# Kernel optimization log

Measured on AMD Instinct MI355X. Metric: run time of the kernel, lower is better.

Reference implementation:

```python
import jax, jax.numpy as jnp
import numpy as np
import math

N_HEADS = 16
DIM_MODEL = 1024
DIM_KQ = 64
DIM_V = 64
B, T = 2, 2048


def setup_inputs() -> dict:
    key = jax.random.key(0)
    ks = jax.random.split(key, 9)
    s = 1.0 / math.sqrt(DIM_MODEL)
    return {
        "x": jax.random.normal(ks[0], (B, T, DIM_MODEL), dtype=jnp.float32),
        "Wq": jax.random.normal(ks[1], (DIM_MODEL, N_HEADS * DIM_KQ), dtype=jnp.float32) * s,
        "bq": jnp.zeros((N_HEADS * DIM_KQ,), dtype=jnp.float32),
        "Wk": jax.random.normal(ks[2], (DIM_MODEL, N_HEADS * DIM_KQ), dtype=jnp.float32) * s,
        "bk": jnp.zeros((N_HEADS * DIM_KQ,), dtype=jnp.float32),
        "Wv": jax.random.normal(ks[3], (DIM_MODEL, N_HEADS * DIM_V), dtype=jnp.float32) * s,
        "bv": jnp.zeros((N_HEADS * DIM_V,), dtype=jnp.float32),
        "Wo": jax.random.normal(ks[4], (N_HEADS * DIM_V, DIM_MODEL), dtype=jnp.float32) * s,
        "bo": jnp.zeros((DIM_MODEL,), dtype=jnp.float32),
    }


def reference(x, Wq, bq, Wk, bk, Wv, bv, Wo, bo):
    b, t, _ = x.shape
    # projections, split into heads: [B, T, h, d]
    q = (x @ Wq + bq).reshape(b, t, N_HEADS, DIM_KQ)
    k = (x @ Wk + bk).reshape(b, t, N_HEADS, DIM_KQ)
    v = (x @ Wv + bv).reshape(b, t, N_HEADS, DIM_V)
    # NOTE: faithful to source einsum 'B Tq h d, B Tk h d -> B h Tk Tq'
    # scores[b, h, tk, tq] = q[b, tq] . k[b, tk]
    scores = jnp.einsum('bqhd,bkhd->bhkq', q, k)
    # softmax over the LAST axis (= query axis tq), as in the source
    attn = jax.nn.softmax(scores / math.sqrt(DIM_KQ), axis=-1)
    # source einsum 'B h Tk Tq, B Tq h dv -> B Tq h dv':
    # sums over Tk only -> out[b, tq, h, dv] = v[b, tq, h, dv] * sum_tk attn[b, h, tk, tq]
    colsum = attn.sum(axis=2)                      # [B, h, Tq]
    mixed = v * colsum.transpose(0, 2, 1)[..., None]  # [B, Tq, h, dv]
    out = mixed.reshape(b, t, N_HEADS * DIM_V) @ Wo + bo
    return out
```

## Files before the change

kernel.cpp:

```cpp
#include <hip/hip_runtime.h>
#include <hip/hip_bf16.h>
#include <stdint.h>

typedef __attribute__((ext_vector_type(4))) float f32x4;
typedef __attribute__((ext_vector_type(8))) __bf16 bf16x8;

#define AS1 __attribute__((address_space(1)))
#define AS3 __attribute__((address_space(3)))

#if __has_builtin(__builtin_amdgcn_exp2f)
#define EXP2(x) __builtin_amdgcn_exp2f(x)
#else
#define EXP2(x) exp2f(x)
#endif

__device__ __forceinline__ ushort f2bf(float f) {
  uint32_t u = __builtin_bit_cast(uint32_t, f);
  u += 0x7fffu + ((u >> 16) & 1u);
  return (ushort)(u >> 16);
}
__device__ __forceinline__ float bf2f(ushort h) {
  uint32_t u = ((uint32_t)h) << 16;
  return __builtin_bit_cast(float, u);
}

#define SCK 0.18033688011112042f

#define GLD(src, dst) \
  __builtin_amdgcn_global_load_lds((const AS1 uint32_t*)(src), (AS3 uint32_t*)(dst), 16, 0, 0)

#define BARRIER()                          \
  do {                                     \
    __builtin_amdgcn_sched_barrier(0);     \
    __builtin_amdgcn_s_barrier();          \
    __builtin_amdgcn_sched_barrier(0);     \
  } while (0)


__global__ void k_cvt_x(const float* __restrict__ x, ushort* __restrict__ xb, int n4) {
  int i = blockIdx.x * blockDim.x + threadIdx.x;
  if (i >= n4) return;
  float4 v = ((const float4*)x)[i];
  ushort4 o;
  o.x = f2bf(v.x); o.y = f2bf(v.y); o.z = f2bf(v.z); o.w = f2bf(v.w);
  ((ushort4*)xb)[i] = o;
}

__global__ void k_prep_w(const float* __restrict__ Wq, const float* __restrict__ Wk,
                         const float* __restrict__ Wv, const float* __restrict__ Wo,
                         ushort* __restrict__ Wt, ushort* __restrict__ Wot) {
  __shared__ float tile[32][33];
  int z = blockIdx.z;
  const float* src = (z == 0) ? Wq : (z == 1) ? Wk : (z == 2) ? Wv : Wo;
  ushort* dst = (z < 3) ? (Wt + (size_t)z * 1048576) : Wot;
  float scale = (z == 1) ? SCK : 1.0f;
  int k0 = blockIdx.y * 32, n0 = blockIdx.x * 32;
  int tx = threadIdx.x, ty = threadIdx.y;
#pragma unroll
  for (int i = 0; i < 4; i++)
    tile[ty + i * 8][tx] = src[(size_t)(k0 + ty + i * 8) * 1024 + n0 + tx];
  __syncthreads();
#pragma unroll
  for (int i = 0; i < 4; i++)
    dst[(size_t)(n0 + ty + i * 8) * 1024 + k0 + tx] = f2bf(tile[tx][ty + i * 8] * scale);
}

template <int MODE>
__global__ __launch_bounds__(512, 2) void k_gemm8(const ushort* __restrict__ A,
                                                  const ushort* __restrict__ Bt,
                                                  void* __restrict__ Cv,
                                                  const float* __restrict__ b0,
                                                  const float* __restrict__ b1,
                                                  const float* __restrict__ b2,
                                                  int K, int ldc) {
  __shared__ char ldsb[131072];
  const int tid = threadIdx.x;
  const int lane = tid & 63;
  const int wid = tid >> 6;
  const int wr = wid >> 2, wc = wid & 3;
  const int l15 = lane & 15, l4 = lane >> 4;
  const int row0 = blockIdx.y * 256;
  const int col0 = blockIdx.x * 256;
  const int T = K >> 5;

  const int swz = ((tid & 3) ^ ((tid >> 3) & 3)) << 3;
  const ushort* Ap = A + (size_t)(row0 + (tid >> 2)) * K + swz;
  const ushort* Bp = Bt + (size_t)(col0 + (tid >> 2)) * K + swz;

#define STAGE_H1(t)                              \
  do {                                           \
    char* bufs = ldsb + (((t) & 3) << 15);       \
    const ushort* pa = Ap + (size_t)(t) * 32;    \
    GLD(pa, bufs + tid * 16);                    \
    GLD(pa + 128 * K, bufs + 8192 + tid * 16);   \
  } while (0)
#define STAGE_H2(t)                              \
  do {                                           \
    char* bufs = ldsb + (((t) & 3) << 15);       \
    const ushort* pb = Bp + (size_t)(t) * 32;    \
    GLD(pb, bufs + 16384 + tid * 16);            \
    GLD(pb + 128 * K, bufs + 24576 + tid * 16);  \
  } while (0)

  int aoffL[8], boffL[4];
#pragma unroll
  for (int m = 0; m < 8; m++) {
    int r = wr * 128 + m * 16 + l15;
    aoffL[m] = r * 64 + ((l4 ^ ((r >> 1) & 3)) << 4);
  }
#pragma unroll
  for (int n = 0; n < 4; n++) {
    int r = wc * 64 + n * 16 + l15;
    boffL[n] = 16384 + r * 64 + ((l4 ^ ((r >> 1) & 3)) << 4);
  }

  f32x4 acc[8][4] = {};

  STAGE_H1(0); STAGE_H2(0);
  STAGE_H1(1); STAGE_H2(1);
  STAGE_H1(2); STAGE_H2(2);
  asm volatile("s_waitcnt vmcnt(8)" ::: "memory");
  BARRIER();

#define PHASE(t, DO_STAGE, VMSTR)                                                     \
  do {                                                                                \
    char* buf = ldsb + (((t) & 3) << 15);                                             \
    {                                                                                 \
      bf16x8 af[4], bfr[4];                                                           \
      _Pragma("unroll") for (int m = 0; m < 4; m++)                                   \
          af[m] = *(const bf16x8*)(buf + aoffL[m]);                                   \
      _Pragma("unroll") for (int n = 0; n < 4; n++)                                   \
          bfr[n] = *(const bf16x8*)(buf + boffL[n]);                                  \
      if (DO_STAGE) STAGE_H1((t) + 3);                                                \
      BARRIER();                                                                      \
      __builtin_amdgcn_s_setprio(1);                                                  \
      _Pragma("unroll") for (int m = 0; m < 4; m++)                                   \
          _Pragma("unroll") for (int n = 0; n < 4; n++)                               \
              acc[m][n] = __builtin_amdgcn_mfma_f32_16x16x32_bf16(af[m], bfr[n],      \
                                                                  acc[m][n], 0, 0, 0);\
      __builtin_amdgcn_s_setprio(0);                                                  \
      BARRIER();                                                                      \
      bf16x8 af2[4];                                                                  \
      _Pragma("unroll") for (int m = 0; m < 4; m++)                                   \
          af2[m] = *(const bf16x8*)(buf + aoffL[m + 4]);                              \
      if (DO_STAGE) STAGE_H2((t) + 3);                                                \
      BARRIER();                                                                      \
      __builtin_amdgcn_s_setprio(1);                                                  \
      _Pragma("unroll") for (int m = 0; m < 4; m++)                                   \
          _Pragma("unroll") for (int n = 0; n < 4; n++)                               \
              acc[m + 4][n] = __builtin_amdgcn_mfma_f32_16x16x32_bf16(                \
                  af2[m], bfr[n], acc[m + 4][n], 0, 0, 0);                            \
      __builtin_amdgcn_s_setprio(0);                                                  \
      asm volatile(VMSTR ::: "memory");                                               \
      BARRIER();                                                                      \
    }                                                                                 \
  } while (0)

  for (int t = 0; t < T - 3; ++t) PHASE(t, true, "s_waitcnt vmcnt(8)");
  PHASE(T - 3, false, "s_waitcnt vmcnt(4)");
  PHASE(T - 2, false, "s_waitcnt vmcnt(0)");
  PHASE(T - 1, false, "s_nop 0");

#undef PHASE
#undef STAGE_H1
#undef STAGE_H2

#pragma unroll
  for (int m = 0; m < 8; m++)
#pragma unroll
    for (int n = 0; n < 4; n++) {
      int colg = col0 + wc * 64 + n * 16 + l15;
      float bias;
      if (MODE == 0) {
        bias = (colg < 1024) ? b0[colg]
                             : ((colg < 2048) ? b1[colg - 1024] * SCK : b2[colg - 2048]);
      } else {
        bias = b0[colg];
      }
#pragma unroll
      for (int j = 0; j < 4; j++) {
        int rowg = row0 + wr * 128 + m * 16 + l4 * 4 + j;
        float v = acc[m][n][j] + bias;
        if (MODE == 0)
          ((ushort*)Cv)[(size_t)rowg * ldc + colg] = f2bf(v);
        else
          ((float*)Cv)[(size_t)rowg * ldc + colg] = v;
      }
    }
}

template <int MODE>
__global__ __launch_bounds__(256) void k_gemm(const ushort* __restrict__ A,
                                              const ushort* __restrict__ Bt,
                                              void* __restrict__ Cv,
                                              const float* __restrict__ b0,
                                              int M, int N, int K, int ldc) {
  __shared__ ushort As[128 * 32];
  __shared__ ushort Bs[128 * 32];
  const int tid = threadIdx.x;
  const int lane = tid & 63;
  const int wid = tid >> 6;
  const int wr = wid >> 1, wc = wid & 1;
  const int row0 = blockIdx.y * 128;
  const int col0 = blockIdx.x * 128;
  const int l15 = lane & 15, l4 = lane >> 4;

  f32x4 acc[4][4] = {};

  for (int k0 = 0; k0 < K; k0 += 32) {
    __syncthreads();
#pragma unroll
    for (int i = 0; i < 2; i++) {
      int c = i * 256 + tid;
      int r = c >> 2, cb = c & 3;
      GLD(A + (size_t)(row0 + r) * K + k0 + cb * 8, (char*)As + c * 16);
      GLD(Bt + (size_t)(col0 + r) * K + k0 + cb * 8, (char*)Bs + c * 16);
    }
    __syncthreads();
    bf16x8 av[4], bv[4];
#pragma unroll
    for (int m = 0; m < 4; m++)
      av[m] = *(const bf16x8*)(As + (wr * 64 + m * 16 + l15) * 32 + l4 * 8);
#pragma unroll
    for (int n = 0; n < 4; n++)
      bv[n] = *(const bf16x8*)(Bs + (wc * 64 + n * 16 + l15) * 32 + l4 * 8);
#pragma unroll
    for (int m = 0; m < 4; m++)
#pragma unroll
      for (int n = 0; n < 4; n++)
        acc[m][n] = __builtin_amdgcn_mfma_f32_16x16x32_bf16(av[m], bv[n], acc[m][n], 0, 0, 0);
  }

#pragma unroll
  for (int m = 0; m < 4; m++)
#pragma unroll
    for (int n = 0; n < 4; n++) {
      int colg = col0 + wc * 64 + n * 16 + l15;
      float bias = b0[colg];
#pragma unroll
      for (int j = 0; j < 4; j++) {
        int rowg = row0 + wr * 64 + m * 16 + l4 * 4 + j;
        float v = acc[m][n][j] + bias;
        if (MODE == 0)
          ((ushort*)Cv)[(size_t)rowg * ldc + colg] = f2bf(v);
        else
          ((float*)Cv)[(size_t)rowg * ldc + colg] = v;
      }
    }
}

__global__ __launch_bounds__(256, 2) void k_attn_z(const ushort* __restrict__ QKV,
                                                   float* __restrict__ Zpart) {
  const int bid = blockIdx.x;
  const int xcd = bid & 7, kk = bid >> 3;
  const int g = xcd * 8 + (kk >> 3);
  const int tkb = kk & 7;
  const int bh = g & 31, s = g >> 5;
  const int b = bh >> 4, h = bh & 15;
  const int tid = threadIdx.x, lane = tid & 63, w = tid >> 6;
  const int l15 = lane & 15, l4 = lane >> 4;
  const size_t rs = 3072;

  __shared__ ushort Ks[256 * 64];
  __shared__ ushort Qs[2][128 * 64];

  const ushort* Kbase = QKV + (size_t)(b * 2048 + tkb * 256) * rs + 1024 + h * 64;
  const ushort* Qbase = QKV + (size_t)(b * 2048 + s * 1024) * rs + h * 64;

  const int csl = ((tid & 7) ^ ((tid >> 3) & 7)) * 8;

#pragma unroll
  for (int i = 0; i < 8; i++) {
    int c = i * 256 + tid;
    GLD(Kbase + (size_t)(c >> 3) * rs + csl, (char*)Ks + c * 16);
  }
  const ushort* gq[4];
#pragma unroll
  for (int i = 0; i < 4; i++) {
    int c = i * 256 + tid;
    gq[i] = Qbase + (size_t)(c >> 3) * rs + csl;
    GLD(gq[i], (char*)Qs[0] + c * 16);
  }
  asm volatile("s_waitcnt vmcnt(0)" ::: "memory");
  BARRIER();

  bf16x8 kf[4][2];
#pragma unroll
  for (int m = 0; m < 4; m++)
#pragma unroll
    for (int d = 0; d < 2; d++) {
      int r = w * 64 + m * 16 + l15;
      kf[m][d] = *(const bf16x8*)((const char*)Ks + r * 128 + (((d * 4 + l4) ^ (r & 7)) << 4));
    }

  float z[4][4] = {};
  const f32x4 zero4 = {0.f, 0.f, 0.f, 0.f};

  for (int t = 0; t < 8; ++t) {
    if (t < 7) {
      char* qd = (char*)Qs[(t + 1) & 1];
#pragma unroll
      for (int i = 0; i < 4; i++) {
        int c = i * 256 + tid;
        GLD(gq[i] + (size_t)(t + 1) * 128 * rs, qd + c * 16);
      }
    }
    const char* qb = (const char*)Qs[t & 1];
    f32x4 acc[4][8];
    __builtin_amdgcn_s_setprio(1);
#pragma unroll
    for (int d = 0; d < 2; d++)
#pragma unroll
      for (int n = 0; n < 8; n++) {
        int r = n * 16 + l15;
        bf16x8 qf = *(const bf16x8*)(qb + r * 128 + (((d * 4 + l4) ^ (r & 7)) << 4));
#pragma unroll
        for (int m = 0; m < 4; m++)
          acc[m][n] = __builtin_amdgcn_mfma_f32_16x16x32_bf16(
              kf[m][d], qf, d == 0 ? zero4 : acc[m][n], 0, 0, 0);
      }
    __builtin_amdgcn_s_setprio(0);
#pragma unroll
    for (int m = 0; m < 4; m++)
#pragma unroll
      for (int n = 0; n < 8; n++)
#pragma unroll
        for (int j = 0; j < 4; j++) z[m][j] += EXP2(acc[m][n][j]);
    if (t < 7) {
      asm volatile("s_waitcnt vmcnt(0)" ::: "memory");
      BARRIER();
    }
  }

#pragma unroll
  for (int m = 0; m < 4; m++)
#pragma unroll
    for (int j = 0; j < 4; j++) {
      float v = z[m][j];
      v += __shfl_xor(v, 1, 64);
      v += __shfl_xor(v, 2, 64);
      v += __shfl_xor(v, 4, 64);
      v += __shfl_xor(v, 8, 64);
      if (l15 == 0)
        Zpart[(size_t)s * 65536 + bh * 2048 + tkb * 256 + w * 64 + m * 16 + l4 * 4 + j] = v;
    }
}

__global__ void k_rz(const float* __restrict__ Zpart, float* __restrict__ rrz) {
  int g = blockIdx.x * 256 + threadIdx.x;
  rrz[g] = 1.0f / (Zpart[g] + Zpart[65536 + g]);
}

__global__ __launch_bounds__(256, 2) void k_attn_cs(const ushort* __restrict__ QKV,
                                                    const float* __restrict__ rrz,
                                                    float* __restrict__ csPart) {
  const int bid = blockIdx.x;
  const int xcd = bid & 7, kk = bid >> 3;
  const int g = xcd * 8 + (kk >> 3);
  const int tqb = kk & 7;
  const int bh = g & 31, s = g >> 5;
  const int b = bh >> 4, h = bh & 15;
  const int tid = threadIdx.x, lane = tid & 63, w = tid >> 6;
  const int l15 = lane & 15, l4 = lane >> 4;
  const size_t rs = 3072;

  __shared__ ushort Qs[256 * 64];
  __shared__ ushort Ks[2][128 * 64];

  const ushort* Qbase = QKV + (size_t)(b * 2048 + tqb * 256) * rs + h * 64;
  const ushort* Kbase = QKV + (size_t)(b * 2048 + s * 1024) * rs + 1024 + h * 64;
  const float* rz0 = rrz + bh * 2048 + s * 1024;

  const int csl = ((tid & 7) ^ ((tid >> 3) & 7)) * 8;

#pragma unroll
  for (int i = 0; i < 8; i++) {
    int c = i * 256 + tid;
    GLD(Qbase + (size_t)(c >> 3) * rs + csl, (char*)Qs + c * 16);
  }
  const ushort* gk[4];
#pragma unroll
  for (int i = 0; i < 4; i++) {
    int c = i * 256 + tid;
    gk[i] = Kbase + (size_t)(c >> 3) * rs + csl;
    GLD(gk[i], (char*)Ks[0] + c * 16);
  }
  asm volatile("s_waitcnt vmcnt(0)" ::: "memory");
  BARRIER();

  bf16x8 qf[4][2];
#pragma unroll
  for (int m = 0; m < 4; m++)
#pragma unroll
    for (int d = 0; d < 2; d++) {
      int r = w * 64 + m * 16 + l15;
      qf[m][d] = *(const bf16x8*)((const char*)Qs + r * 128 + (((d * 4 + l4) ^ (r & 7)) << 4));
    }

  float cs[4][4] = {};
  const f32x4 zero4 = {0.f, 0.f, 0.f, 0.f};

  for (int t = 0; t < 8; ++t) {
    if (t < 7) {
      char* kd = (char*)Ks[(t + 1) & 1];
#pragma unroll
      for (int i = 0; i < 4; i++) {
        int c = i * 256 + tid;
        GLD(gk[i] + (size_t)(t + 1) * 128 * rs, kd + c * 16);
      }
    }
    float rz[8];
#pragma unroll
    for (int n = 0; n < 8; n++) rz[n] = rz0[t * 128 + n * 16 + l15];
    const char* kb = (const char*)Ks[t & 1];
    f32x4 acc[4][8];
    __builtin_amdgcn_s_setprio(1);
#pragma unroll
    for (int d = 0; d < 2; d++)
#pragma unroll
      for (int n = 0; n < 8; n++) {
        int r = n * 16 + l15;
        bf16x8 kft = *(const bf16x8*)(kb + r * 128 + (((d * 4 + l4) ^ (r & 7)) << 4));
#pragma unroll
        for (int m = 0; m < 4; m++)
          acc[m][n] = __builtin_amdgcn_mfma_f32_16x16x32_bf16(
              qf[m][d], kft, d == 0 ? zero4 : acc[m][n], 0, 0, 0);
      }
    __builtin_amdgcn_s_setprio(0);
#pragma unroll
    for (int m = 0; m < 4; m++)
#pragma unroll
      for (int n = 0; n < 8; n++)
#pragma unroll
        for (int j = 0; j < 4; j++)
          cs[m][j] = fmaf(EXP2(acc[m][n][j]), rz[n], cs[m][j]);
    if (t < 7) {
      asm volatile("s_waitcnt vmcnt(0)" ::: "memory");
      BARRIER();
    }
  }

#pragma unroll
  for (int m = 0; m < 4; m++)
#pragma unroll
    for (int j = 0; j < 4; j++) {
      float v = cs[m][j];
      v += __shfl_xor(v, 1, 64);
      v += __shfl_xor(v, 2, 64);
      v += __shfl_xor(v, 4, 64);
      v += __shfl_xor(v, 8, 64);
      if (l15 == 0)
        csPart[(size_t)s * 65536 + bh * 2048 + tqb * 256 + w * 64 + m * 16 + l4 * 4 + j] = v;
    }
}

__global__ void k_mixed(const ushort* __restrict__ QKV, const float* __restrict__ csPart,
                        ushort* __restrict__ mixed) {
  int i = blockIdx.x * 256 + threadIdx.x;
  int row = i >> 7;
  int col = (i & 127) * 8;
  int b = row >> 11, t = row & 2047, h = col >> 6;
  int g = ((b << 4) + h) * 2048 + t;
  float cs = csPart[g] + csPart[65536 + g];
  uint4 raw = *(const uint4*)(QKV + (size_t)row * 3072 + 2048 + col);
  const ushort* pv = (const ushort*)&raw;
  ushort o[8];
#pragma unroll
  for (int k = 0; k < 8; k++) o[k] = f2bf(bf2f(pv[k]) * cs);
  *(uint4*)(mixed + (size_t)row * 1024 + col) = *(uint4*)o;
}


extern "C" void kernel_launch(void* const* d_in, const int* in_sizes, int n_in,
                              void* d_out, int out_size, void* d_ws, size_t ws_size,
                              hipStream_t stream) {
  const float* x = (const float*)d_in[0];
  const float* Wq = (const float*)d_in[1];
  const float* bq = (const float*)d_in[2];
  const float* Wk = (const float*)d_in[3];
  const float* bk = (const float*)d_in[4];
  const float* Wv = (const float*)d_in[5];
  const float* bv = (const float*)d_in[6];
  const float* Wo = (const float*)d_in[7];
  const float* bo = (const float*)d_in[8];

  char* ws = (char*)d_ws;
  ushort* xb     = (ushort*)(ws);
  ushort* Wt     = (ushort*)(ws + 8388608);
  ushort* Wot    = (ushort*)(ws + 14680064);
  ushort* QKV    = (ushort*)(ws + 16777216);
  float* Zpart   = (float*)(ws + 41943040);
  float* rrz     = (float*)(ws + 42467328);
  float* csPart  = (float*)(ws + 42729472);
  ushort* mixed  = (ushort*)(ws + 43253760);

  k_cvt_x<<<4096, 256, 0, stream>>>(x, xb, 4096 * 1024 / 4);
  k_prep_w<<<dim3(32, 32, 4), dim3(32, 8), 0, stream>>>(Wq, Wk, Wv, Wo, Wt, Wot);

  k_gemm8<0><<<dim3(12, 16), 512, 0, stream>>>(xb, Wt, QKV, bq, bk, bv, 1024, 3072);
  k_attn_z<<<512, 256, 0, stream>>>(QKV, Zpart);
  k_rz<<<256, 256, 0, stream>>>(Zpart, rrz);
  k_attn_cs<<<512, 256, 0, stream>>>(QKV, rrz, csPart);
  k_mixed<<<2048, 256, 0, stream>>>(QKV, csPart, mixed);
  k_gemm<1><<<dim3(8, 32), 256, 0, stream>>>(mixed, Wot, d_out, bo, 4096, 1024, 1024, 1024);
}
```

Baseline: 135.5 us.

## Unify GEMMs into one 128x128 BK=64 kernel and triple-buffer attention loads

Replaces the 256x256 four-stage pipelined QKV GEMM and the older output GEMM with a single 128x128-tile kernel. It uses a K-step of 64, XOR-swizzled LDS and a remapped 1D grid for locality. The main loop is no longer software-pipelined: each step loads, waits and then computes. Both attention kernels move from double to triple buffering of the streamed Q/K tiles, so loads are issued two iterations ahead. The new GEMM gives more blocks and lower LDS use but loses global-load/MFMA overlap inside each block.

```diff
diff --git a/kernel.cpp b/kernel.cpp
--- a/kernel.cpp
+++ b/kernel.cpp
@@ -66,107 +66,88 @@
 }
 
 template <int MODE>
-__global__ __launch_bounds__(512, 2) void k_gemm8(const ushort* __restrict__ A,
-                                                  const ushort* __restrict__ Bt,
-                                                  void* __restrict__ Cv,
-                                                  const float* __restrict__ b0,
-                                                  const float* __restrict__ b1,
-                                                  const float* __restrict__ b2,
-                                                  int K, int ldc) {
-  __shared__ char ldsb[131072];
+__global__ __launch_bounds__(256, 3) void k_gemm(const ushort* __restrict__ A,
+                                                 const ushort* __restrict__ Bt,
+                                                 void* __restrict__ Cv,
+                                                 const float* __restrict__ b0,
+                                                 const float* __restrict__ b1,
+                                                 const float* __restrict__ b2,
+                                                 int K, int ldc) {
+  __shared__ ushort As[128 * 64];
+  __shared__ ushort Bs[128 * 64];
   const int tid = threadIdx.x;
   const int lane = tid & 63;
   const int wid = tid >> 6;
-  const int wr = wid >> 2, wc = wid & 3;
+  const int wr = wid >> 1, wc = wid & 1;
   const int l15 = lane & 15, l4 = lane >> 4;
-  const int row0 = blockIdx.y * 256;
-  const int col0 = blockIdx.x * 256;
-  const int T = K >> 5;
-
-  const int swz = ((tid & 3) ^ ((tid >> 3) & 3)) << 3;
-  const ushort* Ap = A + (size_t)(row0 + (tid >> 2)) * K + swz;
-  const ushort* Bp = Bt + (size_t)(col0 + (tid >> 2)) * K + swz;
-
-#define STAGE_H1(t)                              \
-  do {                                           \
-    char* bufs = ldsb + (((t) & 3) << 15);       \
-    const ushort* pa = Ap + (size_t)(t) * 32;    \
-    GLD(pa, bufs + tid * 16);                    \
-    GLD(pa + 128 * K, bufs + 8192 + tid * 16);   \
-  } while (0)
-#define STAGE_H2(t)                              \
-  do {                                           \
-    char* bufs = ldsb + (((t) & 3) << 15);       \
-    const ushort* pb = Bp + (size_t)(t) * 32;    \
-    GLD(pb, bufs + 16384 + tid * 16);            \
-    GLD(pb + 128 * K, bufs + 24576 + tid * 16);  \
-  } while (0)
-
-  int aoffL[8], boffL[4];
-#pragma unroll
-  for (int m = 0; m < 8; m++) {
-    int r = wr * 128 + m * 16 + l15;
-    aoffL[m] = r * 64 + ((l4 ^ ((r >> 1) & 3)) << 4);
+
+  const int chunk = (int)gridDim.x >> 3;
+  const int L = blockIdx.x;
+  const int f = (L & 7) * chunk + (L >> 3);
+  const int row0 = (f & 31) * 128;
+  const int col0 = (f >> 5) * 128;
+  const int T = K >> 6;
+
+  const int rt = tid >> 3;
+  const int cswz = ((tid & 7) ^ (rt & 7)) * 8;
+  const ushort* Ap = A + (size_t)(row0 + rt) * K + cswz;
+  const ushort* Bp = Bt + (size_t)(col0 + rt) * K + cswz;
+
+  int aoff[4][2], boff[4][2];
+#pragma unroll
+  for (int m = 0; m < 4; m++) {
+    int r = wr * 64 + m * 16 + l15;
+#pragma unroll
+    for (int ks = 0; ks < 2; ks++)
+      aoff[m][ks] = r * 128 + (((ks * 4 + l4) ^ (r & 7)) << 4);
   }
 #pragma unroll
   for (int n = 0; n < 4; n++) {
     int r = wc * 64 + n * 16 + l15;
-    boffL[n] = 16384 + r * 64 + ((l4 ^ ((r >> 1) & 3)) << 4);
-  }
-
-  f32x4 acc[8][4] = {};
-
-  STAGE_H1(0); STAGE_H2(0);
-  STAGE_H1(1); STAGE_H2(1);
-  STAGE_H1(2); STAGE_H2(2);
-  asm volatile("s_waitcnt vmcnt(8)" ::: "memory");
-  BARRIER();
-
-#define PHASE(t, DO_STAGE, VMSTR)                                                     \
-  do {                                                                                \
-    char* buf = ldsb + (((t) & 3) << 15);                                             \
-    {                                                                                 \
-      bf16x8 af[4], bfr[4];                                                           \
-      _Pragma("unroll") for (int m = 0; m < 4; m++)                                   \
-          af[m] = *(const bf16x8*)(buf + aoffL[m]);                                   \
-      _Pragma("unroll") for (int n = 0; n < 4; n++)                                   \
-          bfr[n] = *(const bf16x8*)(buf + boffL[n]);                                  \
-      if (DO_STAGE) STAGE_H1((t) + 3);                                                \
-      BARRIER();                                                                      \
-      __builtin_amdgcn_s_setprio(1);                                                  \
-      _Pragma("unroll") for (int m = 0; m < 4; m++)                                   \
-          _Pragma("unroll") for (int n = 0; n < 4; n++)                               \
-              acc[m][n] = __builtin_amdgcn_mfma_f32_16x16x32_bf16(af[m], bfr[n],      \
-                                                                  acc[m][n], 0, 0, 0);\
-      __builtin_amdgcn_s_setprio(0);                                                  \
-      BARRIER();                                                                      \
-      bf16x8 af2[4];                                                                  \
-      _Pragma("unroll") for (int m = 0; m < 4; m++)                                   \
-          af2[m] = *(const bf16x8*)(buf + aoffL[m + 4]);                              \
-      if (DO_STAGE) STAGE_H2((t) + 3);                                                \
-      BARRIER();                                                                      \
-      __builtin_amdgcn_s_setprio(1);                                                  \
-      _Pragma("unroll") for (int m = 0; m < 4; m++)                                   \
-          _Pragma("unroll") for (int n = 0; n < 4; n++)                               \
-              acc[m + 4][n] = __builtin_amdgcn_mfma_f32_16x16x32_bf16(                \
-                  af2[m], bfr[n], acc[m + 4][n], 0, 0, 0);                            \
-      __builtin_amdgcn_s_setprio(0);                                                  \
-      asm volatile(VMSTR ::: "memory");                                               \
-      BARRIER();                                                                      \
-    }                                                                                 \
-  } while (0)
-
-  for (int t = 0; t < T - 3; ++t) PHASE(t, true, "s_waitcnt vmcnt(8)");
-  PHASE(T - 3, false, "s_waitcnt vmcnt(4)");
-  PHASE(T - 2, false, "s_waitcnt vmcnt(0)");
-  PHASE(T - 1, false, "s_nop 0");
-
-#undef PHASE
-#undef STAGE_H1
-#undef STAGE_H2
-
-#pragma unroll
-  for (int m = 0; m < 8; m++)
+#pragma unroll
+    for (int ks = 0; ks < 2; ks++)
+      boff[n][ks] = r * 128 + (((ks * 4 + l4) ^ (r & 7)) << 4);
+  }
+
+  f32x4 acc[4][4] = {};
+
+  for (int t = 0; t < T; ++t) {
+#pragma unroll
+    for (int i = 0; i < 4; i++)
+      GLD(Ap + (size_t)(32 * i) * K + t * 64, (char*)As + (i * 256 + tid) * 16);
+#pragma unroll
+    for (int i = 0; i < 4; i++)
+      GLD(Bp + (size_t)(32 * i) * K + t * 64, (char*)Bs + (i * 256 + tid) * 16);
+    asm volatile("s_waitcnt vmcnt(0)" ::: "memory");
+    BARRIER();
+
+    bf16x8 af[4][2], bf_[4][2];
+#pragma unroll
+    for (int m = 0; m < 4; m++)
+#pragma unroll
+      for (int ks = 0; ks < 2; ks++)
+        af[m][ks] = *(const bf16x8*)((const char*)As + aoff[m][ks]);
+#pragma unroll
+    for (int n = 0; n < 4; n++)
+#pragma unroll
+      for (int ks = 0; ks < 2; ks++)
+        bf_[n][ks] = *(const bf16x8*)((const char*)Bs + boff[n][ks]);
+
+    __builtin_amdgcn_s_setprio(1);
+#pragma unroll
+    for (int m = 0; m < 4; m++)
+#pragma unroll
+      for (int n = 0; n < 4; n++)
+#pragma unroll
+        for (int ks = 0; ks < 2; ks++)
+          acc[m][n] = __builtin_amdgcn_mfma_f32_16x16x32_bf16(af[m][ks], bf_[n][ks],
+                                                              acc[m][n], 0, 0, 0);
+    __builtin_amdgcn_s_setprio(0);
+    BARRIER();
+  }
+
+#pragma unroll
+  for (int m = 0; m < 4; m++)
 #pragma unroll
     for (int n = 0; n < 4; n++) {
       int colg = col0 + wc * 64 + n * 16 + l15;
@@ -177,66 +158,6 @@
       } else {
         bias = b0[colg];
       }
-#pragma unroll
-      for (int j = 0; j < 4; j++) {
-        int rowg = row0 + wr * 128 + m * 16 + l4 * 4 + j;
-        float v = acc[m][n][j] + bias;
-        if (MODE == 0)
-          ((ushort*)Cv)[(size_t)rowg * ldc + colg] = f2bf(v);
-        else
-          ((float*)Cv)[(size_t)rowg * ldc + colg] = v;
-      }
-    }
-}
-
-template <int MODE>
-__global__ __launch_bounds__(256) void k_gemm(const ushort* __restrict__ A,
-                                              const ushort* __restrict__ Bt,
-                                              void* __restrict__ Cv,
-                                              const float* __restrict__ b0,
-                                              int M, int N, int K, int ldc) {
-  __shared__ ushort As[128 * 32];
-  __shared__ ushort Bs[128 * 32];
-  const int tid = threadIdx.x;
-  const int lane = tid & 63;
-  const int wid = tid >> 6;
-  const int wr = wid >> 1, wc = wid & 1;
-  const int row0 = blockIdx.y * 128;
-  const int col0 = blockIdx.x * 128;
-  const int l15 = lane & 15, l4 = lane >> 4;
-
-  f32x4 acc[4][4] = {};
-
-  for (int k0 = 0; k0 < K; k0 += 32) {
-    __syncthreads();
-#pragma unroll
-    for (int i = 0; i < 2; i++) {
-      int c = i * 256 + tid;
-      int r = c >> 2, cb = c & 3;
-      GLD(A + (size_t)(row0 + r) * K + k0 + cb * 8, (char*)As + c * 16);
-      GLD(Bt + (size_t)(col0 + r) * K + k0 + cb * 8, (char*)Bs + c * 16);
-    }
-    __syncthreads();
-    bf16x8 av[4], bv[4];
-#pragma unroll
-    for (int m = 0; m < 4; m++)
-      av[m] = *(const bf16x8*)(As + (wr * 64 + m * 16 + l15) * 32 + l4 * 8);
-#pragma unroll
-    for (int n = 0; n < 4; n++)
-      bv[n] = *(const bf16x8*)(Bs + (wc * 64 + n * 16 + l15) * 32 + l4 * 8);
-#pragma unroll
-    for (int m = 0; m < 4; m++)
-#pragma unroll
-      for (int n = 0; n < 4; n++)
-        acc[m][n] = __builtin_amdgcn_mfma_f32_16x16x32_bf16(av[m], bv[n], acc[m][n], 0, 0, 0);
-  }
-
-#pragma unroll
-  for (int m = 0; m < 4; m++)
-#pragma unroll
-    for (int n = 0; n < 4; n++) {
-      int colg = col0 + wc * 64 + n * 16 + l15;
-      float bias = b0[colg];
 #pragma unroll
       for (int j = 0; j < 4; j++) {
         int rowg = row0 + wr * 64 + m * 16 + l4 * 4 + j;
@@ -262,7 +183,7 @@
   const size_t rs = 3072;
 
   __shared__ ushort Ks[256 * 64];
-  __shared__ ushort Qs[2][128 * 64];
+  __shared__ ushort Qs[3][128 * 64];
 
   const ushort* Kbase = QKV + (size_t)(b * 2048 + tkb * 256) * rs + 1024 + h * 64;
   const ushort* Qbase = QKV + (size_t)(b * 2048 + s * 1024) * rs + h * 64;
@@ -281,7 +202,12 @@
     gq[i] = Qbase + (size_t)(c >> 3) * rs + csl;
     GLD(gq[i], (char*)Qs[0] + c * 16);
   }
-  asm volatile("s_waitcnt vmcnt(0)" ::: "memory");
+#pragma unroll
+  for (int i = 0; i < 4; i++) {
+    int c = i * 256 + tid;
+    GLD(gq[i] + 128 * rs, (char*)Qs[1] + c * 16);
+  }
+  asm volatile("s_waitcnt vmcnt(4)" ::: "memory");
   BARRIER();
 
   bf16x8 kf[4][2];
@@ -297,15 +223,15 @@
   const f32x4 zero4 = {0.f, 0.f, 0.f, 0.f};
 
   for (int t = 0; t < 8; ++t) {
-    if (t < 7) {
-      char* qd = (char*)Qs[(t + 1) & 1];
+    if (t + 2 < 8) {
+      char* qd = (char*)Qs[(t + 2) % 3];
 #pragma unroll
       for (int i = 0; i < 4; i++) {
         int c = i * 256 + tid;
-        GLD(gq[i] + (size_t)(t + 1) * 128 * rs, qd + c * 16);
-      }
-    }
-    const char* qb = (const char*)Qs[t & 1];
+        GLD(gq[i] + (size_t)(t + 2) * 128 * rs, qd + c * 16);
+      }
+    }
+    const char* qb = (const char*)Qs[t % 3];
     f32x4 acc[4][8];
     __builtin_amdgcn_s_setprio(1);
 #pragma unroll
@@ -326,7 +252,10 @@
       for (int n = 0; n < 8; n++)
 #pragma unroll
         for (int j = 0; j < 4; j++) z[m][j] += EXP2(acc[m][n][j]);
-    if (t < 7) {
+    if (t < 6) {
+      asm volatile("s_waitcnt vmcnt(4)" ::: "memory");
+      BARRIER();
+    } else if (t == 6) {
       asm volatile("s_waitcnt vmcnt(0)" ::: "memory");
       BARRIER();
     }
@@ -365,7 +294,7 @@
   const size_t rs = 3072;
 
   __shared__ ushort Qs[256 * 64];
-  __shared__ ushort Ks[2][128 * 64];
+  __shared__ ushort Ks[3][128 * 64];
 
   const ushort* Qbase = QKV + (size_t)(b * 2048 + tqb * 256) * rs + h * 64;
   const ushort* Kbase = QKV + (size_t)(b * 2048 + s * 1024) * rs + 1024 + h * 64;
@@ -385,7 +314,12 @@
     gk[i] = Kbase + (size_t)(c >> 3) * rs + csl;
     GLD(gk[i], (char*)Ks[0] + c * 16);
   }
-  asm volatile("s_waitcnt vmcnt(0)" ::: "memory");
+#pragma unroll
+  for (int i = 0; i < 4; i++) {
+    int c = i * 256 + tid;
+    GLD(gk[i] + 128 * rs, (char*)Ks[1] + c * 16);
+  }
+  asm volatile("s_waitcnt vmcnt(4)" ::: "memory");
   BARRIER();
 
   bf16x8 qf[4][2];
@@ -401,18 +335,18 @@
   const f32x4 zero4 = {0.f, 0.f, 0.f, 0.f};
 
   for (int t = 0; t < 8; ++t) {
-    if (t < 7) {
-      char* kd = (char*)Ks[(t + 1) & 1];
+    float rz[8];
+#pragma unroll
+    for (int n = 0; n < 8; n++) rz[n] = rz0[t * 128 + n * 16 + l15];
+    if (t + 2 < 8) {
+      char* kd = (char*)Ks[(t + 2) % 3];
 #pragma unroll
       for (int i = 0; i < 4; i++) {
         int c = i * 256 + tid;
-        GLD(gk[i] + (size_t)(t + 1) * 128 * rs, kd + c * 16);
-      }
-    }
-    float rz[8];
-#pragma unroll
-    for (int n = 0; n < 8; n++) rz[n] = rz0[t * 128 + n * 16 + l15];
-    const char* kb = (const char*)Ks[t & 1];
+        GLD(gk[i] + (size_t)(t + 2) * 128 * rs, kd + c * 16);
+      }
+    }
+    const char* kb = (const char*)Ks[t % 3];
     f32x4 acc[4][8];
     __builtin_amdgcn_s_setprio(1);
 #pragma unroll
@@ -434,7 +368,10 @@
 #pragma unroll
         for (int j = 0; j < 4; j++)
           cs[m][j] = fmaf(EXP2(acc[m][n][j]), rz[n], cs[m][j]);
-    if (t < 7) {
+    if (t < 6) {
+      asm volatile("s_waitcnt vmcnt(4)" ::: "memory");
+      BARRIER();
+    } else if (t == 6) {
       asm volatile("s_waitcnt vmcnt(0)" ::: "memory");
       BARRIER();
     }
@@ -497,10 +434,10 @@
   k_cvt_x<<<4096, 256, 0, stream>>>(x, xb, 4096 * 1024 / 4);
   k_prep_w<<<dim3(32, 32, 4), dim3(32, 8), 0, stream>>>(Wq, Wk, Wv, Wo, Wt, Wot);
 
-  k_gemm8<0><<<dim3(12, 16), 512, 0, stream>>>(xb, Wt, QKV, bq, bk, bv, 1024, 3072);
+  k_gemm<0><<<768, 256, 0, stream>>>(xb, Wt, QKV, bq, bk, bv, 1024, 3072);
   k_attn_z<<<512, 256, 0, stream>>>(QKV, Zpart);
   k_rz<<<256, 256, 0, stream>>>(Zpart, rrz);
   k_attn_cs<<<512, 256, 0, stream>>>(QKV, rrz, csPart);
   k_mixed<<<2048, 256, 0, stream>>>(QKV, csPart, mixed);
-  k_gemm<1><<<dim3(8, 32), 256, 0, stream>>>(mixed, Wot, d_out, bo, 4096, 1024, 1024, 1024);
-}
+  k_gemm<1><<<256, 256, 0, stream>>>(mixed, Wot, d_out, bo, nullptr, nullptr, 1024, 1024);
+}
```

After: 124.1 us. 1.09x faster.
